# Performance work log

Hardware: AMD Instinct MI355X
Metric: run time of the kernel (lower is better)

The kernel has to match this reference:

```python
import jax, jax.numpy as jnp
import numpy as np

FEAT = 32      # feature_dim
NA = 64        # num_azimuths
NE = 32        # num_elevations - 2 (interior elevation rings)
N = 2_000_000  # number of query points
NORMALIZED = False


def setup_inputs() -> dict:
    key = jax.random.key(0)
    k1, k2, k3 = jax.random.split(key, 3)
    u = jax.random.uniform(k1, (2, N), dtype=jnp.float32)
    # azimuth in [-pi, pi), elevation in [-pi/2, pi/2]
    az = u[0] * (2.0 * np.pi) * (1.0 - 1e-7) - np.pi
    el = u[1] * np.pi - np.pi / 2
    points_to_interp = jnp.stack([az, el])
    grid_values = jax.random.normal(k2, (FEAT, NA, NE), dtype=jnp.float32) * 0.1
    grid_values_poles = jax.random.normal(k3, (FEAT, 2), dtype=jnp.float32) * 0.1
    return {
        "points_to_interp": points_to_interp,
        "grid_values": grid_values,
        "grid_values_poles": grid_values_poles,
    }


def _slerp(f1, f2, theta, omega, normalized):
    # spherical linear interpolation weights; omega is a static python float
    w1 = jnp.sin(omega - theta)
    w2 = jnp.sin(theta)
    if normalized:
        s = w1 + w2
        w1 = w1 / s
        w2 = w2 / s
    else:
        so = np.sin(omega)
        w1 = w1 / so
        w2 = w2 / so
    return w1 * f1 + w2 * f2


def reference(points_to_interp, grid_values, grid_values_poles):
    F, na, ne = grid_values.shape
    # static grid ticks (buffers in the torch module)
    ticks_az = jnp.asarray(np.linspace(-np.pi, np.pi, na + 1)[:-1], jnp.float32)
    ticks_el = jnp.asarray(np.linspace(-np.pi / 2, np.pi / 2, ne + 2)[1:-1], jnp.float32)
    omega_az = 2.0 * np.pi / na            # azimuth tick spacing
    omega_el = np.pi / (ne + 1)            # elevation tick spacing (incl. poles)

    az = points_to_interp[0]
    el = points_to_interp[1]

    # torch.bucketize(right=False) == searchsorted side='left'
    ar = jnp.searchsorted(ticks_az, az, side="left")
    al = ar - 1
    ar = jnp.where(ar >= na, 0, ar)        # azimuth wraps around
    al = jnp.where(al < 0, na - 1, al)     # torch negative index wrap

    er = jnp.searchsorted(ticks_el, el, side="left")
    south = er == 0                        # below lowest interior ring
    north = er == ne                       # above highest interior ring
    eil = jnp.clip(er - 1, 0, ne - 1)      # lower ring index (clamped)
    eir = jnp.clip(er, 0, ne - 1)          # upper ring index (clamped)

    # azimuth slerp on the lower and upper rings (4 gathers of [F, N])
    theta_az = az - ticks_az[al]
    f_b = _slerp(grid_values[:, al, eil], grid_values[:, ar, eil], theta_az, omega_az, NORMALIZED)
    f_t = _slerp(grid_values[:, al, eir], grid_values[:, ar, eir], theta_az, omega_az, NORMALIZED)

    # pole regions: blend ring value with pole feature.
    # slerp(a, b, theta, omega) == slerp(b, a, omega - theta, omega), so the
    # north-pole branch slerp(pole, f_top_ring, pi/2 - el) equals
    # slerp(f_top_ring, pole, el - ticks_el[ne-1]) with the same omega_el.
    f1 = jnp.where(south, grid_values_poles[:, 0:1], f_b)
    f2 = jnp.where(north, grid_values_poles[:, 1:2], f_t)
    base = jnp.where(south, -np.pi / 2, ticks_el[eil])
    theta_el = el - base
    return _slerp(f1, f2, theta_el, omega_el, NORMALIZED)
```

## Files before the change

kernel.cpp:

```cpp
#include <hip/hip_runtime.h>
#include <hip/hip_fp16.h>

namespace {

constexpr int kFeat = 32;
constexpr int kNA = 64;
constexpr int kNE = 32;
constexpr int kGridElems = kFeat * kNA * kNE;
constexpr int kPoleElems = kFeat * 2;
constexpr int kCols = kNA * kNE;
constexpr int kColS = kCols;
constexpr int kColN = kCols + 1;
constexpr int kTotCols = kCols + 2;

constexpr float kPi  = 3.14159265358979323846f;
constexpr float kPi2 = 1.57079632679489661923f;
constexpr float kOmegaAz = 0.09817477042468103f;
constexpr float kOmegaEl = 0.09519977738150889f;
constexpr float kInvOmegaAz = 10.18591635788130f;
constexpr float kInvOmegaEl = 10.50422624406509f;
constexpr float kInvSinAz = 10.20229703f;
constexpr float kInvSinEl = 10.52010966f;

__global__ __launch_bounds__(256) void transpose_grid_h(
    const float* __restrict__ g, const float* __restrict__ poles,
    __half* __restrict__ gt) {
  int idx = blockIdx.x * 256 + threadIdx.x;
  if (idx < kGridElems) {
    int f = idx >> 11;
    int ae = idx & 2047;
    gt[ae * kFeat + f] = __float2half(g[idx]);
  }
  if (idx < kPoleElems) {
    int f = idx >> 1;
    int p = idx & 1;
    gt[(kCols + p) * kFeat + f] = __float2half(poles[idx]);
  }
}

struct PointSetup {
  int col_bl, col_br, col_tl, col_tr;
  float a1, a2, b1, b2;
};

__device__ __forceinline__ PointSetup setup_point(float az, float el) {
  PointSetup s;
  float ta = (az + kPi) * kInvOmegaAz;
  int ar0 = (int)ceilf(ta);
  int al = ar0 - 1;
  int ar = (ar0 >= kNA) ? 0 : ar0;
  if (al < 0) al = kNA - 1;
  float theta_a = az - (-kPi + (float)al * kOmegaAz);
  float w1a = __sinf(kOmegaAz - theta_a) * kInvSinAz;
  float w2a = __sinf(theta_a) * kInvSinAz;

  float ue = (el + kPi2) * kInvOmegaEl;
  int er = (int)ceilf(ue) - 1;
  er = min(max(er, 0), kNE);
  bool south = (er == 0);
  bool north = (er == kNE);
  int eil = min(max(er - 1, 0), kNE - 1);
  int eir = min(er, kNE - 1);
  float base = south ? -kPi2 : (-kPi2 + (float)(eil + 1) * kOmegaEl);
  float theta_e = el - base;
  float w1e = __sinf(kOmegaEl - theta_e) * kInvSinEl;
  float w2e = __sinf(theta_e) * kInvSinEl;

  s.col_bl = al * kNE + eil;
  s.col_br = ar * kNE + eil;
  s.col_tl = al * kNE + eir;
  s.col_tr = ar * kNE + eir;
  s.a1 = w1e * w1a; s.a2 = w1e * w2a;
  s.b1 = w2e * w1a; s.b2 = w2e * w2a;
  if (south) {
    s.col_bl = kColS; s.col_br = kColS;
    s.a1 = 0.5f * w1e; s.a2 = s.a1;
  }
  if (north) {
    s.col_tl = kColN; s.col_tr = kColN;
    s.b1 = 0.5f * w2e; s.b2 = s.b1;
  }
  return s;
}

__global__ __launch_bounds__(256) void interp_h(
    const float* __restrict__ pts, const __half* __restrict__ gt,
    float* __restrict__ out, int n) {
  int slot = blockIdx.x * 256 + threadIdx.x;
  int i = slot >> 2;
  int j = slot & 3;
  if (i >= n) return;
  float az = pts[i];
  float el = pts[n + i];
  PointSetup s = setup_point(az, el);

  union H8 { uint4 u; __half2 h[4]; };
  H8 bl, br, tl, tr;
  int off = j * 8;
  bl.u = *(const uint4*)(gt + s.col_bl * kFeat + off);
  br.u = *(const uint4*)(gt + s.col_br * kFeat + off);
  tl.u = *(const uint4*)(gt + s.col_tl * kFeat + off);
  tr.u = *(const uint4*)(gt + s.col_tr * kFeat + off);

  float acc[8];
#pragma unroll
  for (int q = 0; q < 4; ++q) {
    float2 vbl = __half22float2(bl.h[q]);
    float2 vbr = __half22float2(br.h[q]);
    float2 vtl = __half22float2(tl.h[q]);
    float2 vtr = __half22float2(tr.h[q]);
    acc[2 * q + 0] = s.a1 * vbl.x + s.a2 * vbr.x + s.b1 * vtl.x + s.b2 * vtr.x;
    acc[2 * q + 1] = s.a1 * vbl.y + s.a2 * vbr.y + s.b1 * vtl.y + s.b2 * vtr.y;
  }

  size_t sn = (size_t)n;
  float* o = out + (size_t)(8 * j) * sn + i;
#pragma unroll
  for (int k = 0; k < 8; ++k) o[(size_t)k * sn] = acc[k];
}

__global__ __launch_bounds__(256) void interp_d(
    const float* __restrict__ pts, const float* __restrict__ g,
    const float* __restrict__ poles, float* __restrict__ out, int n) {
  int i = blockIdx.x * 256 + threadIdx.x;
  if (i >= n) return;
  float az = pts[i];
  float el = pts[n + i];
  PointSetup s = setup_point(az, el);

  float a1 = s.a1, a2 = s.a2, b1 = s.b1, b2 = s.b2;
  float pw0 = 0.0f, pw1 = 0.0f;
  if (s.col_bl == kColS) { pw0 = a1 + a2; a1 = 0.0f; a2 = 0.0f; }
  if (s.col_tl == kColN) { pw1 = b1 + b2; b1 = 0.0f; b2 = 0.0f; }

  const float* gbl = g + (s.col_bl < kCols ? s.col_bl : 0);
  const float* gbr = g + (s.col_br < kCols ? s.col_br : 0);
  const float* gtl = g + (s.col_tl < kCols ? s.col_tl : 0);
  const float* gtr = g + (s.col_tr < kCols ? s.col_tr : 0);
  size_t sn = (size_t)n;
#pragma unroll 8
  for (int f = 0; f < kFeat; ++f) {
    float v = a1 * gbl[f * kCols] + a2 * gbr[f * kCols]
            + b1 * gtl[f * kCols] + b2 * gtr[f * kCols]
            + pw0 * poles[f * 2 + 0] + pw1 * poles[f * 2 + 1];
    out[(size_t)f * sn + i] = v;
  }
}

}

extern "C" void kernel_launch(void* const* d_in, const int* in_sizes, int n_in,
                              void* d_out, int out_size, void* d_ws, size_t ws_size,
                              hipStream_t stream) {
  (void)n_in; (void)out_size;
  const float* pts   = (const float*)d_in[0];
  const float* grid  = (const float*)d_in[1];
  const float* poles = (const float*)d_in[2];
  float* out = (float*)d_out;
  int n = in_sizes[0] / 2;

  size_t need = (size_t)(kTotCols * kFeat) * sizeof(__half);
  if (ws_size >= need) {
    __half* gt = (__half*)d_ws;
    transpose_grid_h<<<(kGridElems + 255) / 256, 256, 0, stream>>>(grid, poles, gt);
    long long slots = 4LL * n;
    int blocks = (int)((slots + 255) / 256);
    interp_h<<<blocks, 256, 0, stream>>>(pts, gt, out, n);
  } else {
    int blocks = (n + 255) / 256;
    interp_d<<<blocks, 256, 0, stream>>>(pts, grid, poles, out, n);
  }
}
```

Baseline: 311.6 us.

## Process four slots per thread with double-buffered gathers in interp kernel

Each thread now handles four (point, feature-chunk) slots strided by the total thread count, and it launches a quarter as many blocks. Gathers for the next slot are issued before computing and storing the current one, using two register buffers, so memory latency overlaps with arithmetic and stores. This raises register use and may lower occupancy. The strided mapping keeps stores coalesced within each pass.

```diff
diff --git a/kernel.cpp b/kernel.cpp
--- a/kernel.cpp
+++ b/kernel.cpp
@@ -83,25 +83,23 @@
   return s;
 }
 
-__global__ __launch_bounds__(256) void interp_h(
-    const float* __restrict__ pts, const __half* __restrict__ gt,
-    float* __restrict__ out, int n) {
-  int slot = blockIdx.x * 256 + threadIdx.x;
-  int i = slot >> 2;
-  int j = slot & 3;
-  if (i >= n) return;
-  float az = pts[i];
-  float el = pts[n + i];
-  PointSetup s = setup_point(az, el);
-
+__device__ __forceinline__ void gather_cols(
+    const __half* __restrict__ gt, const PointSetup& s, int j,
+    uint4& bl, uint4& br, uint4& tl, uint4& tr) {
+  int off = j * 8;
+  bl = *(const uint4*)(gt + s.col_bl * kFeat + off);
+  br = *(const uint4*)(gt + s.col_br * kFeat + off);
+  tl = *(const uint4*)(gt + s.col_tl * kFeat + off);
+  tr = *(const uint4*)(gt + s.col_tr * kFeat + off);
+}
+
+__device__ __forceinline__ void compute_store(
+    const PointSetup& s, const uint4& blu, const uint4& bru,
+    const uint4& tlu, const uint4& tru, int i, int j,
+    float* __restrict__ out, size_t sn) {
   union H8 { uint4 u; __half2 h[4]; };
   H8 bl, br, tl, tr;
-  int off = j * 8;
-  bl.u = *(const uint4*)(gt + s.col_bl * kFeat + off);
-  br.u = *(const uint4*)(gt + s.col_br * kFeat + off);
-  tl.u = *(const uint4*)(gt + s.col_tl * kFeat + off);
-  tr.u = *(const uint4*)(gt + s.col_tr * kFeat + off);
-
+  bl.u = blu; br.u = bru; tl.u = tlu; tr.u = tru;
   float acc[8];
 #pragma unroll
   for (int q = 0; q < 4; ++q) {
@@ -112,11 +110,52 @@
     acc[2 * q + 0] = s.a1 * vbl.x + s.a2 * vbr.x + s.b1 * vtl.x + s.b2 * vtr.x;
     acc[2 * q + 1] = s.a1 * vbl.y + s.a2 * vbr.y + s.b1 * vtl.y + s.b2 * vtr.y;
   }
-
-  size_t sn = (size_t)n;
   float* o = out + (size_t)(8 * j) * sn + i;
 #pragma unroll
   for (int k = 0; k < 8; ++k) o[(size_t)k * sn] = acc[k];
+}
+
+constexpr int kPPT = 4;
+
+__global__ __launch_bounds__(256) void interp_h(
+    const float* __restrict__ pts, const __half* __restrict__ gt,
+    float* __restrict__ out, int n) {
+  const long long T = (long long)gridDim.x * 256;
+  const long long t0 = (long long)blockIdx.x * 256 + threadIdx.x;
+  const long long nslots = 4LL * n;
+  const size_t sn = (size_t)n;
+
+  const long long sA = t0;
+  const long long sB = t0 + T;
+  const long long sC = t0 + 2 * T;
+  const long long sD = t0 + 3 * T;
+  const bool vA = sA < nslots, vB = sB < nslots, vC = sC < nslots, vD = sD < nslots;
+  const int iA = (int)(sA >> 2), jA = (int)(sA & 3);
+  const int iB = (int)(sB >> 2), jB = (int)(sB & 3);
+  const int iC = (int)(sC >> 2), jC = (int)(sC & 3);
+  const int iD = (int)(sD >> 2), jD = (int)(sD & 3);
+
+  float azA = 0.f, elA = 0.f, azB = 0.f, elB = 0.f;
+  float azC = 0.f, elC = 0.f, azD = 0.f, elD = 0.f;
+  if (vA) { azA = pts[iA]; elA = pts[n + iA]; }
+  if (vB) { azB = pts[iB]; elB = pts[n + iB]; }
+  if (vC) { azC = pts[iC]; elC = pts[n + iC]; }
+  if (vD) { azD = pts[iD]; elD = pts[n + iD]; }
+
+  PointSetup st0, st1;
+  uint4 bl0, br0, tl0, tr0, bl1, br1, tl1, tr1;
+
+  if (vA) { st0 = setup_point(azA, elA); gather_cols(gt, st0, jA, bl0, br0, tl0, tr0); }
+  if (vB) { st1 = setup_point(azB, elB); gather_cols(gt, st1, jB, bl1, br1, tl1, tr1); }
+
+  if (vA) compute_store(st0, bl0, br0, tl0, tr0, iA, jA, out, sn);
+  if (vC) { st0 = setup_point(azC, elC); gather_cols(gt, st0, jC, bl0, br0, tl0, tr0); }
+
+  if (vB) compute_store(st1, bl1, br1, tl1, tr1, iB, jB, out, sn);
+  if (vD) { st1 = setup_point(azD, elD); gather_cols(gt, st1, jD, bl1, br1, tl1, tr1); }
+
+  if (vC) compute_store(st0, bl0, br0, tl0, tr0, iC, jC, out, sn);
+  if (vD) compute_store(st1, bl1, br1, tl1, tr1, iD, jD, out, sn);
 }
 
 __global__ __launch_bounds__(256) void interp_d(
@@ -164,7 +203,8 @@
     __half* gt = (__half*)d_ws;
     transpose_grid_h<<<(kGridElems + 255) / 256, 256, 0, stream>>>(grid, poles, gt);
     long long slots = 4LL * n;
-    int blocks = (int)((slots + 255) / 256);
+    long long threads = (slots + kPPT - 1) / kPPT;
+    int blocks = (int)((threads + 255) / 256);
     interp_h<<<blocks, 256, 0, stream>>>(pts, gt, out, n);
   } else {
     int blocks = (n + 255) / 256;
```

Result: no change. 316.1 us (+1.4%).

## Stage half-precision grid in LDS with persistent blocks and prefetched point loads

Applied to the files above, without the earlier changes.

Replaces the one-slot-per-thread interpolation kernel with a persistent kernel of 256 blocks of 1024 threads. Each block first copies the whole fp16 transposed grid (about 131 KB) into shared memory, then loops over a contiguous chunk of slots while prefetching the next point's coordinates. The four corner gathers now read LDS instead of global/L2 memory. The cost is a large LDS footprint that allows only one block per CU, a per-block fill of the table, a fixed grid size, and a chunk layout in which consecutive threads of a wave still write separate output rows.

```diff
diff --git a/kernel.cpp b/kernel.cpp
--- a/kernel.cpp
+++ b/kernel.cpp
@@ -12,6 +12,8 @@
 constexpr int kColS = kCols;
 constexpr int kColN = kCols + 1;
 constexpr int kTotCols = kCols + 2;
+constexpr int kLdsHalfs = kTotCols * kFeat;
+constexpr int kLdsVec = kLdsHalfs / 8;
 
 constexpr float kPi  = 3.14159265358979323846f;
 constexpr float kPi2 = 1.57079632679489661923f;
@@ -83,25 +85,13 @@
   return s;
 }
 
-__global__ __launch_bounds__(256) void interp_h(
-    const float* __restrict__ pts, const __half* __restrict__ gt,
-    float* __restrict__ out, int n) {
-  int slot = blockIdx.x * 256 + threadIdx.x;
-  int i = slot >> 2;
-  int j = slot & 3;
-  if (i >= n) return;
-  float az = pts[i];
-  float el = pts[n + i];
-  PointSetup s = setup_point(az, el);
-
+__device__ __forceinline__ void compute_store(
+    const PointSetup& s, const uint4& blu, const uint4& bru,
+    const uint4& tlu, const uint4& tru, int i, int j,
+    float* __restrict__ out, size_t sn) {
   union H8 { uint4 u; __half2 h[4]; };
   H8 bl, br, tl, tr;
-  int off = j * 8;
-  bl.u = *(const uint4*)(gt + s.col_bl * kFeat + off);
-  br.u = *(const uint4*)(gt + s.col_br * kFeat + off);
-  tl.u = *(const uint4*)(gt + s.col_tl * kFeat + off);
-  tr.u = *(const uint4*)(gt + s.col_tr * kFeat + off);
-
+  bl.u = blu; br.u = bru; tl.u = tlu; tr.u = tru;
   float acc[8];
 #pragma unroll
   for (int q = 0; q < 4; ++q) {
@@ -112,11 +102,53 @@
     acc[2 * q + 0] = s.a1 * vbl.x + s.a2 * vbr.x + s.b1 * vtl.x + s.b2 * vtr.x;
     acc[2 * q + 1] = s.a1 * vbl.y + s.a2 * vbr.y + s.b1 * vtl.y + s.b2 * vtr.y;
   }
-
-  size_t sn = (size_t)n;
   float* o = out + (size_t)(8 * j) * sn + i;
 #pragma unroll
   for (int k = 0; k < 8; ++k) o[(size_t)k * sn] = acc[k];
+}
+
+__global__ __launch_bounds__(1024) void interp_lds(
+    const float* __restrict__ pts, const __half* __restrict__ gt,
+    float* __restrict__ out, int n, long long chunk) {
+  __shared__ __half lds[kLdsHalfs];
+  {
+    const uint4* src = (const uint4*)gt;
+    uint4* dst = (uint4*)lds;
+    for (int t = threadIdx.x; t < kLdsVec; t += 1024) dst[t] = src[t];
+  }
+  __syncthreads();
+
+  const long long nslots = 4LL * n;
+  long long base = (long long)blockIdx.x * chunk;
+  long long end = base + chunk;
+  if (end > nslots) end = nslots;
+  const size_t sn = (size_t)n;
+
+  long long slot = base + threadIdx.x;
+  float az = 0.f, el = 0.f;
+  if (slot < end) {
+    int i = (int)(slot >> 2);
+    az = pts[i];
+    el = pts[n + i];
+  }
+  while (slot < end) {
+    const long long next = slot + 1024;
+    const int i = (int)(slot >> 2);
+    const int j = (int)(slot & 3);
+    PointSetup s = setup_point(az, el);
+    const int off = j * 8;
+    uint4 bl = *(const uint4*)(lds + s.col_bl * kFeat + off);
+    uint4 br = *(const uint4*)(lds + s.col_br * kFeat + off);
+    uint4 tl = *(const uint4*)(lds + s.col_tl * kFeat + off);
+    uint4 tr = *(const uint4*)(lds + s.col_tr * kFeat + off);
+    if (next < end) {
+      int i2 = (int)(next >> 2);
+      az = pts[i2];
+      el = pts[n + i2];
+    }
+    compute_store(s, bl, br, tl, tr, i, j, out, sn);
+    slot = next;
+  }
 }
 
 __global__ __launch_bounds__(256) void interp_d(
@@ -163,9 +195,11 @@
   if (ws_size >= need) {
     __half* gt = (__half*)d_ws;
     transpose_grid_h<<<(kGridElems + 255) / 256, 256, 0, stream>>>(grid, poles, gt);
-    long long slots = 4LL * n;
-    int blocks = (int)((slots + 255) / 256);
-    interp_h<<<blocks, 256, 0, stream>>>(pts, gt, out, n);
+    const long long slots = 4LL * n;
+    const int blocks = 256;
+    long long chunk =
+        ((slots + (long long)blocks * 64 - 1) / ((long long)blocks * 64)) * 64;
+    interp_lds<<<blocks, 1024, 0, stream>>>(pts, gt, out, n, chunk);
   } else {
     int blocks = (n + 255) / 256;
     interp_d<<<blocks, 256, 0, stream>>>(pts, grid, poles, out, n);
```

After: 343.2 us. 1.1x slower.

## Stage interpolated outputs in shared memory for coalesced 16-byte stores

Applied to the files above, without the earlier changes.

Each block now processes a tile of 256 points with 4 feature-slices per point, writing results into a shared-memory tile laid out feature-major. After a barrier, the tile is written out as 16-byte vector stores along contiguous point ranges per feature row. Previously each thread wrote 8 scalar floats strided by n, with only 4-byte contiguity across lanes that were spaced by point index. This trades 32KB of shared memory per block (lower occupancy) and a sync for wider, better-coalesced global writes of the 256MB output.

```diff
diff --git a/kernel.cpp b/kernel.cpp
--- a/kernel.cpp
+++ b/kernel.cpp
@@ -83,40 +83,88 @@
   return s;
 }
 
-__global__ __launch_bounds__(256) void interp_h(
+constexpr int kTile = 256;
+constexpr int kTileFloats = kFeat * kTile;
+
+__global__ __launch_bounds__(256) void interp_t(
     const float* __restrict__ pts, const __half* __restrict__ gt,
     float* __restrict__ out, int n) {
-  int slot = blockIdx.x * 256 + threadIdx.x;
-  int i = slot >> 2;
-  int j = slot & 3;
-  if (i >= n) return;
-  float az = pts[i];
-  float el = pts[n + i];
-  PointSetup s = setup_point(az, el);
-
-  union H8 { uint4 u; __half2 h[4]; };
-  H8 bl, br, tl, tr;
-  int off = j * 8;
-  bl.u = *(const uint4*)(gt + s.col_bl * kFeat + off);
-  br.u = *(const uint4*)(gt + s.col_br * kFeat + off);
-  tl.u = *(const uint4*)(gt + s.col_tl * kFeat + off);
-  tr.u = *(const uint4*)(gt + s.col_tr * kFeat + off);
-
-  float acc[8];
-#pragma unroll
-  for (int q = 0; q < 4; ++q) {
-    float2 vbl = __half22float2(bl.h[q]);
-    float2 vbr = __half22float2(br.h[q]);
-    float2 vtl = __half22float2(tl.h[q]);
-    float2 vtr = __half22float2(tr.h[q]);
-    acc[2 * q + 0] = s.a1 * vbl.x + s.a2 * vbr.x + s.b1 * vtl.x + s.b2 * vtr.x;
-    acc[2 * q + 1] = s.a1 * vbl.y + s.a2 * vbr.y + s.b1 * vtl.y + s.b2 * vtr.y;
-  }
-
-  size_t sn = (size_t)n;
-  float* o = out + (size_t)(8 * j) * sn + i;
-#pragma unroll
-  for (int k = 0; k < 8; ++k) o[(size_t)k * sn] = acc[k];
+  __shared__ float tile[kTileFloats];
+  const int base = blockIdx.x * kTile;
+  const int rem = min(kTile, n - base);
+  const size_t sn = (size_t)n;
+  const int t = threadIdx.x;
+
+  int   pidx[4];
+  float azv[4], elv[4];
+#pragma unroll
+  for (int c = 0; c < 4; ++c) {
+    int L = t + 256 * c;
+    int p = L >> 2;
+    pidx[c] = p;
+    if (p < rem) {
+      int i = base + p;
+      azv[c] = pts[i];
+      elv[c] = pts[n + i];
+    } else {
+      azv[c] = 0.f; elv[c] = 0.f;
+    }
+  }
+
+#pragma unroll
+  for (int c = 0; c < 4; ++c) {
+    int L = t + 256 * c;
+    int p = pidx[c];
+    int j = L & 3;
+    if (p < rem) {
+      PointSetup s = setup_point(azv[c], elv[c]);
+      union H8 { uint4 u; __half2 h[4]; };
+      H8 bl, br, tl, tr;
+      const int off = j * 8;
+      bl.u = *(const uint4*)(gt + s.col_bl * kFeat + off);
+      br.u = *(const uint4*)(gt + s.col_br * kFeat + off);
+      tl.u = *(const uint4*)(gt + s.col_tl * kFeat + off);
+      tr.u = *(const uint4*)(gt + s.col_tr * kFeat + off);
+
+      float* dst = tile + (8 * j) * kTile + p;
+#pragma unroll
+      for (int q = 0; q < 4; ++q) {
+        float2 vbl = __half22float2(bl.h[q]);
+        float2 vbr = __half22float2(br.h[q]);
+        float2 vtl = __half22float2(tl.h[q]);
+        float2 vtr = __half22float2(tr.h[q]);
+        dst[(2 * q + 0) * kTile] =
+            s.a1 * vbl.x + s.a2 * vbr.x + s.b1 * vtl.x + s.b2 * vtr.x;
+        dst[(2 * q + 1) * kTile] =
+            s.a1 * vbl.y + s.a2 * vbr.y + s.b1 * vtl.y + s.b2 * vtr.y;
+      }
+    }
+  }
+
+  __syncthreads();
+
+  if (rem == kTile) {
+    const uint4* src = (const uint4*)tile;
+#pragma unroll
+    for (int r = 0; r < 8; ++r) {
+      int u = t + 256 * r;
+      int row = u >> 6;
+      int col = u & 63;
+      *(uint4*)(out + (size_t)row * sn + base + 4 * col) = src[u];
+    }
+  } else {
+    for (int r = 0; r < 8; ++r) {
+      int u = t + 256 * r;
+      int row = u >> 6;
+      int col4 = (u & 63) * 4;
+      if (col4 < rem) {
+        int m = min(4, rem - col4);
+        const float* s4 = tile + row * kTile + col4;
+        float* o = out + (size_t)row * sn + base + col4;
+        for (int e = 0; e < m; ++e) o[e] = s4[e];
+      }
+    }
+  }
 }
 
 __global__ __launch_bounds__(256) void interp_d(
@@ -163,9 +211,8 @@
   if (ws_size >= need) {
     __half* gt = (__half*)d_ws;
     transpose_grid_h<<<(kGridElems + 255) / 256, 256, 0, stream>>>(grid, poles, gt);
-    long long slots = 4LL * n;
-    int blocks = (int)((slots + 255) / 256);
-    interp_h<<<blocks, 256, 0, stream>>>(pts, gt, out, n);
+    int blocks = (n + kTile - 1) / kTile;
+    interp_t<<<blocks, 256, 0, stream>>>(pts, gt, out, n);
   } else {
     int blocks = (n + 255) / 256;
     interp_d<<<blocks, 256, 0, stream>>>(pts, grid, poles, out, n);
```

After: 292.3 us. -6.2%, faster.
